# Optimization experiments

Hardware: AMD Instinct MI355X
Metric: run time of the kernel (lower is better)

The kernel has to match this reference:

```python
import jax, jax.numpy as jnp
import numpy as np

B, S, D = 2, 2048, 1024
H, DH = 16, 64
C = 64          # chunk_size (sliding window)
WF = 4          # widening factor
FMIN = jnp.finfo(jnp.float32).min


def _ln(x, scale, offset, eps=1e-5):
    mu = jnp.mean(x, axis=-1, keepdims=True)
    var = jnp.var(x, axis=-1, keepdims=True)
    return (x - mu) * jax.lax.rsqrt(var + eps) * scale + offset


def setup_inputs() -> dict:
    key = jax.random.key(0)
    ks = jax.random.split(key, 12)
    std = 0.02
    inp = {
        'x': jax.random.normal(ks[0], (B, S, D), dtype=jnp.float32),
        'causal_mask': jnp.tril(jnp.ones((S, S), dtype=bool))[None, None],  # (1,1,S,S)
        'pos': jax.random.normal(ks[1], (C, D), dtype=jnp.float32),          # pos_0..pos_{C-1}
        'rpe': std * jax.random.normal(ks[2], (H, C), dtype=jnp.float32),
        'Wq': std * jax.random.normal(ks[3], (D, H * DH), dtype=jnp.float32),
        'Wk': std * jax.random.normal(ks[4], (D, H * DH), dtype=jnp.float32),
        'Wv': std * jax.random.normal(ks[5], (D, H * DH), dtype=jnp.float32),
        'Wo': std * jax.random.normal(ks[6], (H * DH, D), dtype=jnp.float32),
        'ln1_scale': jnp.ones((D,), jnp.float32),
        'ln1_offset': jnp.zeros((D,), jnp.float32),
        'W1': std * jax.random.normal(ks[7], (D, WF * D), dtype=jnp.float32),
        'b1': jnp.zeros((WF * D,), jnp.float32),
        'W2': std * jax.random.normal(ks[8], (WF * D, D), dtype=jnp.float32),
        'b2': jnp.zeros((D,), jnp.float32),
        'ln2_scale': jnp.ones((D,), jnp.float32),
        'ln2_offset': jnp.zeros((D,), jnp.float32),
    }
    return inp


def _sliding_window_mask(rpe, seq_len):
    # mask[h,t,T] = rpe[h, t-T] if 0 <= t-T < C (lower diagonals), else -inf
    d = jnp.arange(seq_len)[:, None] - jnp.arange(seq_len)[None, :]  # (S,S)
    valid = (d >= 0) & (d < C)
    dc = jnp.clip(d, 0, C - 1)
    val = jnp.where(valid[None], rpe[:, dc], 0.0)  # (H,S,S)
    return jnp.where(val != 0, val, FMIN)


def reference(x, causal_mask, pos, rpe, Wq, Wk, Wv, Wo, ln1_scale, ln1_offset,
              W1, b1, W2, b2, ln2_scale, ln2_offset):
    seq_len = x.shape[1]
    # front/rear positional vectors: pos_i added at positions i, i+C, i+2C, ...
    h = x + pos[jnp.arange(seq_len) % C]  # (B,S,D)

    q = (h @ Wq).reshape(B, seq_len, H, DH)
    k = (h @ Wk).reshape(B, seq_len, H, DH)
    v = (h @ Wv).reshape(B, seq_len, H, DH)

    attn = jnp.einsum('bthd,bThd->bhtT', q, k) * (1.0 / jnp.sqrt(DH))
    attn = attn + _sliding_window_mask(rpe, seq_len)[None]  # learned diag bias
    attn = jnp.where(causal_mask, attn, FMIN)
    attn = jax.nn.softmax(attn, axis=-1)

    out = jnp.einsum('bhtT,bThd->bthd', attn, v).reshape(B, seq_len, H * DH)
    out = out @ Wo

    # dropout_prob = 0 -> identity
    attention = _ln(h + out, ln1_scale, ln1_offset)
    ff = jax.nn.relu(attention @ W1 + b1) @ W2 + b2
    return _ln(ff + attention, ln2_scale, ln2_offset)
```

## Files before the change

### kernel.cpp

```cpp
#include <hip/hip_runtime.h>
#include <hip/hip_bf16.h>

#define DEVI static __device__ __forceinline__

typedef __attribute__((ext_vector_type(4))) float f32x4;
typedef __attribute__((ext_vector_type(8))) short bf16x8;
typedef __attribute__((ext_vector_type(4))) short s16x4;

constexpr int TB  = 2;
constexpr int TS  = 2048;
constexpr int TD  = 1024;
constexpr int TH  = 16;
constexpr int TDH = 64;
constexpr int TC  = 64;
constexpr int TFF = 4096;
constexpr int TM  = TB * TS;

DEVI float bf2f(short s) {
  return __builtin_bit_cast(float, (unsigned)((unsigned short)s) << 16);
}
DEVI short f2bf(float f) {
  return __builtin_bit_cast(short, __float2bfloat16(f));
}

#define GLD16(gp, lp)                                              \
  __builtin_amdgcn_global_load_lds(                                \
      (const __attribute__((address_space(1))) void*)(gp),         \
      (__attribute__((address_space(3))) void*)(lp), 16, 0, 0)

#define WAITVM(N) asm volatile("s_waitcnt vmcnt(" #N ")" ::: "memory")

__global__ __launch_bounds__(256) void k_trans_all(
    const float* __restrict__ Wq, const float* __restrict__ Wk,
    const float* __restrict__ Wv, const float* __restrict__ Wo,
    const float* __restrict__ W1, const float* __restrict__ W2,
    __hip_bfloat16* __restrict__ WqkvT, __hip_bfloat16* __restrict__ WoT,
    __hip_bfloat16* __restrict__ W1T, __hip_bfloat16* __restrict__ W2T) {
  __shared__ float tile[32][33];
  int bid = blockIdx.x;
  const float* src; __hip_bfloat16* dst;
  int K, N, n0, k0;
  if (bid < 4096) {
    int m = bid >> 10, t = bid & 1023;
    src = (m == 0) ? Wq : (m == 1) ? Wk : (m == 2) ? Wv : Wo;
    dst = (m == 3) ? WoT : WqkvT + (size_t)m * TD * TD;
    K = TD; N = TD; n0 = (t & 31) * 32; k0 = (t >> 5) * 32;
  } else if (bid < 8192) {
    int t = bid - 4096;
    src = W1; dst = W1T; K = TD; N = TFF;
    n0 = (t & 127) * 32; k0 = (t >> 7) * 32;
  } else {
    int t = bid - 8192;
    src = W2; dst = W2T; K = TFF; N = TD;
    n0 = (t & 31) * 32; k0 = (t >> 5) * 32;
  }
  int tx = threadIdx.x & 31, ty = threadIdx.x >> 5;
  for (int i = 0; i < 32; i += 8)
    tile[ty + i][tx] = src[(size_t)(k0 + ty + i) * N + n0 + tx];
  __syncthreads();
  for (int i = 0; i < 32; i += 8)
    dst[(size_t)(n0 + ty + i) * K + k0 + tx] = __float2bfloat16(tile[tx][ty + i]);
}

__global__ __launch_bounds__(256) void k_addpos(
    const float* __restrict__ x, const float* __restrict__ pos,
    __hip_bfloat16* __restrict__ hb, int total4) {
  int i = blockIdx.x * 256 + threadIdx.x;
  if (i >= total4) return;
  int e = i * 4;
  int d = e & (TD - 1);
  int t = (e / TD) & (TS - 1);
  f32x4 xv = *(const f32x4*)(x + e);
  f32x4 pv = *(const f32x4*)(pos + (size_t)(t & (TC - 1)) * TD + d);
  s16x4 hb4;
  for (int j = 0; j < 4; j++) hb4[j] = f2bf(xv[j] + pv[j]);
  *(s16x4*)((short*)hb + e) = hb4;
}

template <int BN, int EPI>
__global__ __launch_bounds__(512, 2) void k_gemm8(
    const __hip_bfloat16* __restrict__ A, const __hip_bfloat16* __restrict__ BT,
    void* __restrict__ Cout, const float* __restrict__ bias,
    int M, int N, int K, int lda, int ldb) {
  constexpr int BM = 256, BK = 32;
  constexpr int FN = BN / 64;
  __shared__ __align__(16) short As[4][BM * BK];
  __shared__ __align__(16) short Bs[4][BN * BK];
  int tid = threadIdx.x, lane = tid & 63, wave = tid >> 6;
  int wm = wave >> 2, wn = wave & 3;
  int fr = lane & 15, fg = lane >> 4;
  int m0 = blockIdx.x * BM, n0 = blockIdx.y * BN;
  size_t koff = (size_t)blockIdx.z * K;
  const short* Ab = (const short*)A + koff;
  const short* Bb = (const short*)BT + koff;

  int r0 = tid >> 2, s0 = (tid & 3) ^ ((r0 >> 1) & 3);
  int r1 = 128 + r0, s1 = (tid & 3) ^ ((r1 >> 1) & 3);
  const short* pA0 = Ab + (size_t)(m0 + r0) * lda + s0 * 8;
  const short* pA1 = Ab + (size_t)(m0 + r1) * lda + s1 * 8;
  const short* pB0 = Bb + (size_t)(n0 + r0) * ldb + s0 * 8;
  const short* pB1 = (BN == 256) ? Bb + (size_t)(n0 + r1) * ldb + s1 * 8 : pB0;
  int dst0 = (wave * 64) * 16;
  int dst1 = (512 + wave * 64) * 16;

  auto stageA = [&](int d, int T) {
    GLD16(pA0 + T * BK, (char*)&As[d][0] + dst0);
    GLD16(pA1 + T * BK, (char*)&As[d][0] + dst1);
  };
  auto stageB = [&](int d, int T) {
    GLD16(pB0 + T * BK, (char*)&Bs[d][0] + dst0);
    if constexpr (BN == 256) GLD16(pB1 + T * BK, (char*)&Bs[d][0] + dst1);
  };

  f32x4 acc[8][FN];
#pragma unroll
  for (int m = 0; m < 8; m++)
#pragma unroll
    for (int n = 0; n < FN; n++) acc[m][n] = f32x4{0.f, 0.f, 0.f, 0.f};

  const int nt = K / BK;
  stageA(0, 0); stageB(0, 0);
  stageA(1, 1); stageB(1, 1);
  stageA(2, 2); stageB(2, 2);
  if (BN == 256) { WAITVM(8); } else { WAITVM(6); }
  __builtin_amdgcn_s_barrier();

  for (int t = 0; t < nt; t++) {
    int d = t & 3, pf = (t + 3) & 3;
    bool dopf = (t + 3) < nt;
    const char* Al = (const char*)&As[d][0];
    const char* Bl = (const char*)&Bs[d][0];
    if constexpr (BN == 256) {
      bf16x8 a[4], b[4];
#pragma unroll
      for (int mt = 0; mt < 4; mt++) {
        int row = wm * 128 + mt * 16 + fr;
        a[mt] = *(const bf16x8*)(Al + row * 64 + ((fg ^ ((row >> 1) & 3)) << 4));
      }
#pragma unroll
      for (int n = 0; n < 4; n++) {
        int row = wn * 64 + n * 16 + fr;
        b[n] = *(const bf16x8*)(Bl + row * 64 + ((fg ^ ((row >> 1) & 3)) << 4));
      }
      if (dopf) stageA(pf, t + 3);
      __builtin_amdgcn_s_barrier();
      __builtin_amdgcn_s_setprio(1);
#pragma unroll
      for (int mt = 0; mt < 4; mt++)
#pragma unroll
        for (int n = 0; n < 4; n++)
          acc[mt][n] = __builtin_amdgcn_mfma_f32_16x16x32_bf16(a[mt], b[n],
                                                               acc[mt][n], 0, 0, 0);
      __builtin_amdgcn_s_setprio(0);
      __builtin_amdgcn_s_barrier();
#pragma unroll
      for (int mt = 0; mt < 4; mt++) {
        int row = wm * 128 + 64 + mt * 16 + fr;
        a[mt] = *(const bf16x8*)(Al + row * 64 + ((fg ^ ((row >> 1) & 3)) << 4));
      }
      if (dopf) stageB(pf, t + 3);
      if (t < nt - 3) { WAITVM(8); }
      else if (t == nt - 3) { WAITVM(4); }
      else if (t == nt - 2) { WAITVM(0); }
      __builtin_amdgcn_s_barrier();
      __builtin_amdgcn_s_setprio(1);
#pragma unroll
      for (int mt = 0; mt < 4; mt++)
#pragma unroll
        for (int n = 0; n < 4; n++)
          acc[4 + mt][n] = __builtin_amdgcn_mfma_f32_16x16x32_bf16(a[mt], b[n],
                                                                   acc[4 + mt][n], 0, 0, 0);
      __builtin_amdgcn_s_setprio(0);
      __builtin_amdgcn_s_barrier();
    } else {
      bf16x8 a[8], b[2];
#pragma unroll
      for (int mt = 0; mt < 8; mt++) {
        int row = wm * 128 + mt * 16 + fr;
        a[mt] = *(const bf16x8*)(Al + row * 64 + ((fg ^ ((row >> 1) & 3)) << 4));
      }
#pragma unroll
      for (int n = 0; n < 2; n++) {
        int row = wn * 32 + n * 16 + fr;
        b[n] = *(const bf16x8*)(Bl + row * 64 + ((fg ^ ((row >> 1) & 3)) << 4));
      }
      if (dopf) { stageA(pf, t + 3); stageB(pf, t + 3); }
      if (t < nt - 3) { WAITVM(6); }
      else if (t == nt - 3) { WAITVM(3); }
      else if (t == nt - 2) { WAITVM(0); }
      __builtin_amdgcn_s_barrier();
      __builtin_amdgcn_s_setprio(1);
#pragma unroll
      for (int mt = 0; mt < 8; mt++)
#pragma unroll
        for (int n = 0; n < 2; n++)
          acc[mt][n] = __builtin_amdgcn_mfma_f32_16x16x32_bf16(a[mt], b[n],
                                                               acc[mt][n], 0, 0, 0);
      __builtin_amdgcn_s_setprio(0);
      __builtin_amdgcn_s_barrier();
    }
  }

  float* Cf = (float*)Cout + (size_t)blockIdx.z * M * N;
#pragma unroll
  for (int mt = 0; mt < 8; mt++)
#pragma unroll
    for (int n = 0; n < FN; n++) {
      int col = n0 + wn * (BN / 4) + n * 16 + fr;
      float bv = (EPI == 1) ? bias[col] : 0.f;
#pragma unroll
      for (int j = 0; j < 4; j++) {
        int row = m0 + wm * 128 + mt * 16 + fg * 4 + j;
        float v = acc[mt][n][j];
        if (EPI == 1) { v += bv; v = fmaxf(v, 0.f); }
        if (EPI == 2)
          Cf[(size_t)row * N + col] = v;
        else
          ((__hip_bfloat16*)Cout)[(size_t)row * N + col] = __float2bfloat16(v);
      }
    }
}

__global__ __launch_bounds__(256) void k_vtrans(
    const __hip_bfloat16* __restrict__ qkv, __hip_bfloat16* __restrict__ vT) {
  __shared__ short tile[64][68];
  int bh = blockIdx.x;
  int tb = blockIdx.y;
  int b = bh >> 4, h = bh & 15;
  int tid = threadIdx.x;
#pragma unroll
  for (int i = 0; i < 2; i++) {
    int c = i * 256 + tid;
    int trow = c >> 3, seg = c & 7;
    bf16x8 v = *(const bf16x8*)((const short*)qkv +
        (size_t)(b * TS + tb * 64 + trow) * 3072 + 2048 + h * TDH + seg * 8);
    s16x4 lo = {v[0], v[1], v[2], v[3]}, hi = {v[4], v[5], v[6], v[7]};
    *(s16x4*)&tile[trow][seg * 8] = lo;
    *(s16x4*)&tile[trow][seg * 8 + 4] = hi;
  }
  __syncthreads();
#pragma unroll
  for (int i2 = 0; i2 < 2; i2++) {
    int c = i2 * 256 + tid;
    int d = c >> 3, ts = c & 7;
    bf16x8 o;
#pragma unroll
    for (int j = 0; j < 8; j++) o[j] = tile[ts * 8 + j][d];
    *(bf16x8*)((short*)vT + (size_t)bh * TDH * TS + (size_t)d * TS +
               tb * 64 + ts * 8) = o;
  }
}

__global__ __launch_bounds__(256) void k_attn(
    const __hip_bfloat16* __restrict__ qkv, const __hip_bfloat16* __restrict__ vT,
    const float* __restrict__ rpe, __hip_bfloat16* __restrict__ out) {
  __shared__ __align__(16) short K_lds[128 * 64];
  __shared__ __align__(16) short VT_lds[64 * 128];
  __shared__ __align__(16) short P_lds[4][16 * 136];
  __shared__ float rpe_lds[TC];
  int tid = threadIdx.x, lane = tid & 63, wave = tid >> 6;
  int fr = lane & 15, g = lane >> 4;
  int blk = blockIdx.x;
  int qt = blk & 31, bh = blk >> 5;
  int h = bh & 15, b = bh >> 4;
  int t0 = qt * 64;
  const short* qg = (const short*)qkv;

  if (tid < TC) rpe_lds[tid] = rpe[h * TC + tid];

#pragma unroll
  for (int i = 0; i < 4; i++) {
    int cb = i * 256 + wave * 64;
    int c = cb + lane;
    int row = c >> 3, slot = c & 7;
    int seg = slot ^ (row & 7);
    int kr = t0 - 64 + row; if (kr < 0) kr = 0;
    GLD16(qg + ((size_t)(b * TS + kr) * 3072 + 1024 + h * TDH + seg * 8),
          (char*)K_lds + cb * 16);
  }
  const short* vg = (const short*)vT + (size_t)bh * TDH * TS;
#pragma unroll
  for (int i = 0; i < 4; i++) {
    int cb = i * 256 + wave * 64;
    int c = cb + lane;
    int row = c >> 4, slot = c & 15;
    int seg = slot ^ (row & 15);
    int tc = t0 - 64 + seg * 8; if (tc < 0) tc = 0;
    GLD16(vg + (size_t)row * TS + tc, (char*)VT_lds + cb * 16);
  }

  int qrow = t0 + wave * 16 + fr;
  const short* qptr = qg + ((size_t)(b * TS + qrow) * 3072 + h * TDH + g * 8);
  bf16x8 qf0 = *(const bf16x8*)qptr;
  bf16x8 qf1 = *(const bf16x8*)(qptr + 32);

  __syncthreads();

  f32x4 S[8] = {};
#pragma unroll
  for (int kk = 0; kk < 2; kk++) {
    bf16x8 a = kk ? qf1 : qf0;
#pragma unroll
    for (int nt = 0; nt < 8; nt++) {
      int row = nt * 16 + fr;
      int slot = (kk * 4 + g) ^ (row & 7);
      bf16x8 bfrag = *(const bf16x8*)((const char*)K_lds + row * 128 + slot * 16);
      S[nt] = __builtin_amdgcn_mfma_f32_16x16x32_bf16(a, bfrag, S[nt], 0, 0, 0);
    }
  }

  int wq = wave * 16;
#pragma unroll
  for (int r = 0; r < 4; r++) {
    int ql = g * 4 + r;
    float sc[8];
    float m = -3.4028235e38f;
#pragma unroll
    for (int nt = 0; nt < 8; nt++) {
      int jj = nt * 16 + fr;
      int d = wq + ql + 64 - jj;
      bool valid = (d >= 0) && (d < TC) && (t0 - 64 + jj >= 0);
      float v = valid ? (S[nt][r] * 0.125f + rpe_lds[d & (TC - 1)])
                      : -3.4028235e38f;
      sc[nt] = v;
      m = fmaxf(m, v);
    }
#pragma unroll
    for (int o = 1; o < 16; o <<= 1) m = fmaxf(m, __shfl_xor(m, o));
    float p[8], sum = 0.f;
#pragma unroll
    for (int nt = 0; nt < 8; nt++) { p[nt] = __expf(sc[nt] - m); sum += p[nt]; }
#pragma unroll
    for (int o = 1; o < 16; o <<= 1) sum += __shfl_xor(sum, o);
    float rs = 1.0f / sum;
#pragma unroll
    for (int nt = 0; nt < 8; nt++)
      P_lds[wave][ql * 136 + nt * 16 + fr] = f2bf(p[nt] * rs);
  }

  f32x4 O[4] = {};
#pragma unroll
  for (int kk = 0; kk < 4; kk++) {
    bf16x8 pa = *(const bf16x8*)((const char*)&P_lds[wave][0] +
                                 fr * 272 + kk * 64 + g * 16);
#pragma unroll
    for (int dt = 0; dt < 4; dt++) {
      int row = dt * 16 + fr;
      int slot = (kk * 4 + g) ^ (row & 15);
      bf16x8 vb = *(const bf16x8*)((const char*)VT_lds + row * 256 + slot * 16);
      O[dt] = __builtin_amdgcn_mfma_f32_16x16x32_bf16(pa, vb, O[dt], 0, 0, 0);
    }
  }

  size_t ob = ((size_t)(b * TS + t0 + wq + g * 4)) * TD + h * TDH;
#pragma unroll
  for (int dt = 0; dt < 4; dt++)
#pragma unroll
    for (int r = 0; r < 4; r++)
      ((short*)out)[ob + (size_t)r * TD + dt * 16 + fr] = f2bf(O[dt][r]);
}

DEVI float block_sum(float v, float* red) {
  for (int o = 32; o; o >>= 1) v += __shfl_xor(v, o);
  int wave = threadIdx.x >> 6;
  if ((threadIdx.x & 63) == 0) red[wave] = v;
  __syncthreads();
  float r = red[0] + red[1] + red[2] + red[3];
  __syncthreads();
  return r;
}

__global__ __launch_bounds__(256) void k_ln1(
    const float* __restrict__ x, const float* __restrict__ pos,
    const float* __restrict__ P0, const float* __restrict__ P1,
    const float* __restrict__ scale, const float* __restrict__ offset,
    float* __restrict__ outf, __hip_bfloat16* __restrict__ outb) {
  __shared__ float red[4];
  int row = blockIdx.x, tid = threadIdx.x;
  int t = row & (TS - 1), pr = t & (TC - 1);
  size_t base = (size_t)row * TD + tid * 4;
  f32x4 xv = *(const f32x4*)(x + base);
  f32x4 pv = *(const f32x4*)(pos + (size_t)pr * TD + tid * 4);
  f32x4 a0 = *(const f32x4*)(P0 + base);
  f32x4 a1 = *(const f32x4*)(P1 + base);
  xv = xv + pv + a0 + a1;
  float s = xv[0] + xv[1] + xv[2] + xv[3];
  s = block_sum(s, red);
  float mu = s * (1.f / TD);
  float s2 = 0.f;
  for (int j = 0; j < 4; j++) { float dlt = xv[j] - mu; s2 += dlt * dlt; }
  s2 = block_sum(s2, red);
  float rs = rsqrtf(s2 * (1.f / TD) + 1e-5f);
  f32x4 sc = *(const f32x4*)(scale + tid * 4);
  f32x4 of = *(const f32x4*)(offset + tid * 4);
  f32x4 y;
  for (int j = 0; j < 4; j++) y[j] = (xv[j] - mu) * rs * sc[j] + of[j];
  *(f32x4*)(outf + base) = y;
  s16x4 pb;
  for (int j = 0; j < 4; j++) pb[j] = f2bf(y[j]);
  *(s16x4*)((short*)outb + base) = pb;
}

__global__ __launch_bounds__(256) void k_ln2(
    const float* __restrict__ P0, const float* __restrict__ P1,
    const float* __restrict__ R, const float* __restrict__ bias,
    const float* __restrict__ scale, const float* __restrict__ offset,
    float* __restrict__ outf) {
  __shared__ float red[4];
  int row = blockIdx.x, tid = threadIdx.x;
  size_t base = (size_t)row * TD + tid * 4;
  f32x4 a0 = *(const f32x4*)(P0 + base);
  f32x4 a1 = *(const f32x4*)(P1 + base);
  f32x4 rv = *(const f32x4*)(R + base);
  f32x4 bi = *(const f32x4*)(bias + tid * 4);
  f32x4 xv = a0 + a1 + rv + bi;
  float s = xv[0] + xv[1] + xv[2] + xv[3];
  s = block_sum(s, red);
  float mu = s * (1.f / TD);
  float s2 = 0.f;
  for (int j = 0; j < 4; j++) { float dlt = xv[j] - mu; s2 += dlt * dlt; }
  s2 = block_sum(s2, red);
  float rs = rsqrtf(s2 * (1.f / TD) + 1e-5f);
  f32x4 sc = *(const f32x4*)(scale + tid * 4);
  f32x4 of = *(const f32x4*)(offset + tid * 4);
  f32x4 y;
  for (int j = 0; j < 4; j++) y[j] = (xv[j] - mu) * rs * sc[j] + of[j];
  *(f32x4*)(outf + base) = y;
}

extern "C" void kernel_launch(void* const* d_in, const int* in_sizes, int n_in,
                              void* d_out, int out_size, void* d_ws, size_t ws_size,
                              hipStream_t stream) {
  const float* x    = (const float*)d_in[0];
  const float* pos  = (const float*)d_in[2];
  const float* rpe  = (const float*)d_in[3];
  const float* Wq   = (const float*)d_in[4];
  const float* Wk   = (const float*)d_in[5];
  const float* Wv   = (const float*)d_in[6];
  const float* Wo   = (const float*)d_in[7];
  const float* ln1s = (const float*)d_in[8];
  const float* ln1o = (const float*)d_in[9];
  const float* W1   = (const float*)d_in[10];
  const float* b1   = (const float*)d_in[11];
  const float* W2   = (const float*)d_in[12];
  const float* b2   = (const float*)d_in[13];
  const float* ln2s = (const float*)d_in[14];
  const float* ln2o = (const float*)d_in[15];

  char* ws = (char*)d_ws;
  const size_t MB = 1ull << 20;
  __hip_bfloat16* WqkvT = (__hip_bfloat16*)(ws + 0 * MB);
  __hip_bfloat16* WoT   = (__hip_bfloat16*)(ws + 6 * MB);
  __hip_bfloat16* W1T   = (__hip_bfloat16*)(ws + 8 * MB);
  __hip_bfloat16* W2T   = (__hip_bfloat16*)(ws + 16 * MB);
  __hip_bfloat16* hB    = (__hip_bfloat16*)(ws + 24 * MB);
  __hip_bfloat16* qkv   = (__hip_bfloat16*)(ws + 32 * MB);
  __hip_bfloat16* aoB   = (__hip_bfloat16*)(ws + 56 * MB);
  float*          oF2   = (float*)(ws + 64 * MB);
  float*          atF   = (float*)(ws + 96 * MB);
  __hip_bfloat16* atB   = (__hip_bfloat16*)(ws + 24 * MB);
  __hip_bfloat16* ff1   = (__hip_bfloat16*)(ws + 32 * MB);
  float*          ff2   = (float*)(ws + 64 * MB);
  __hip_bfloat16* vTb   = (__hip_bfloat16*)(ws + 112 * MB);

  dim3 blk(256), blk5(512);

  k_trans_all<<<12288, blk, 0, stream>>>(Wq, Wk, Wv, Wo, W1, W2,
                                         WqkvT, WoT, W1T, W2T);

  k_addpos<<<(TM * TD / 4 + 255) / 256, blk, 0, stream>>>(x, pos, hB, TM * TD / 4);

  k_gemm8<256, 0><<<dim3(TM / 256, 3072 / 256, 1), blk5, 0, stream>>>(
      hB, WqkvT, qkv, nullptr, TM, 3072, TD, TD, TD);

  k_vtrans<<<dim3(TB * TH, TS / 64), blk, 0, stream>>>(qkv, vTb);
  k_attn<<<TB * TH * (TS / 64), blk, 0, stream>>>(qkv, vTb, rpe, aoB);

  k_gemm8<128, 2><<<dim3(TM / 256, TD / 128, 2), blk5, 0, stream>>>(
      aoB, WoT, oF2, nullptr, TM, TD, TD / 2, TD, TD);

  k_ln1<<<TM, blk, 0, stream>>>(x, pos, oF2, oF2 + (size_t)TM * TD, ln1s, ln1o, atF, atB);

  k_gemm8<256, 1><<<dim3(TM / 256, TFF / 256, 1), blk5, 0, stream>>>(
      atB, W1T, ff1, b1, TM, TFF, TD, TD, TD);

  k_gemm8<128, 2><<<dim3(TM / 256, TD / 128, 2), blk5, 0, stream>>>(
      ff1, W2T, ff2, nullptr, TM, TD, TFF / 2, TFF, TFF);

  k_ln2<<<TM, blk, 0, stream>>>(ff2, ff2 + (size_t)TM * TD, atF, b2, ln2s, ln2o,
                                (float*)d_out);
}
```

Measured before the change: 204.9 us.

## Restructure GEMM main loop with one barrier per tile and B-fragment double buffering

Rewrites the bf16 MFMA GEMM pipeline so each K-tile needs one barrier instead of two or three. B fragments for the next tile are read from LDS into registers ahead of time while the current tile computes. Prefetch issue is now unified and happens after the barrier. For BN=128 the wave grid changes from 2x4 to 4x2 (64x64 per wave) to balance A and B fragment reuse. The extra live registers for the next B fragments could raise pressure under the 512-thread, 2-block launch bound.

After: 238.7 us. 16.5% more time.

```diff
diff --git a/kernel.cpp b/kernel.cpp
--- a/kernel.cpp
+++ b/kernel.cpp
@@ -78,16 +78,18 @@
 }
 
 template <int BN, int EPI>
-__global__ __launch_bounds__(512, 2) void k_gemm8(
+__global__ __launch_bounds__(512, 2) void k_gemm9(
     const __hip_bfloat16* __restrict__ A, const __hip_bfloat16* __restrict__ BT,
     void* __restrict__ Cout, const float* __restrict__ bias,
     int M, int N, int K, int lda, int ldb) {
   constexpr int BM = 256, BK = 32;
-  constexpr int FN = BN / 64;
+  constexpr int MT  = (BN == 256) ? 8 : 4;
+  constexpr int WMR = (BN == 256) ? 128 : 64;
   __shared__ __align__(16) short As[4][BM * BK];
   __shared__ __align__(16) short Bs[4][BN * BK];
   int tid = threadIdx.x, lane = tid & 63, wave = tid >> 6;
-  int wm = wave >> 2, wn = wave & 3;
+  int wm = (BN == 256) ? (wave >> 2) : (wave >> 1);
+  int wn = (BN == 256) ? (wave & 3) : (wave & 1);
   int fr = lane & 15, fg = lane >> 4;
   int m0 = blockIdx.x * BM, n0 = blockIdx.y * BN;
   size_t koff = (size_t)blockIdx.z * K;
@@ -103,114 +105,84 @@
   int dst0 = (wave * 64) * 16;
   int dst1 = (512 + wave * 64) * 16;
 
-  auto stageA = [&](int d, int T) {
+  auto stage = [&](int d, int T) {
     GLD16(pA0 + T * BK, (char*)&As[d][0] + dst0);
     GLD16(pA1 + T * BK, (char*)&As[d][0] + dst1);
-  };
-  auto stageB = [&](int d, int T) {
     GLD16(pB0 + T * BK, (char*)&Bs[d][0] + dst0);
     if constexpr (BN == 256) GLD16(pB1 + T * BK, (char*)&Bs[d][0] + dst1);
   };
-
-  f32x4 acc[8][FN];
-#pragma unroll
-  for (int m = 0; m < 8; m++)
-#pragma unroll
-    for (int n = 0; n < FN; n++) acc[m][n] = f32x4{0.f, 0.f, 0.f, 0.f};
+  auto readB = [&](int d, bf16x8* b) {
+#pragma unroll
+    for (int n = 0; n < 4; n++) {
+      int row = wn * 64 + n * 16 + fr;
+      b[n] = *(const bf16x8*)((const char*)&Bs[d][0] + row * 64 +
+                              ((fg ^ ((row >> 1) & 3)) << 4));
+    }
+  };
+
+  f32x4 acc[MT][4];
+#pragma unroll
+  for (int m = 0; m < MT; m++)
+#pragma unroll
+    for (int n = 0; n < 4; n++) acc[m][n] = f32x4{0.f, 0.f, 0.f, 0.f};
 
   const int nt = K / BK;
-  stageA(0, 0); stageB(0, 0);
-  stageA(1, 1); stageB(1, 1);
-  stageA(2, 2); stageB(2, 2);
-  if (BN == 256) { WAITVM(8); } else { WAITVM(6); }
+  stage(0, 0);
+  stage(1, 1);
+  if (BN == 256) { WAITVM(4); } else { WAITVM(3); }
   __builtin_amdgcn_s_barrier();
+  asm volatile("" ::: "memory");
+  stage(2, 2);
+
+  bf16x8 bcur[4], bnxt[4];
+  readB(0, bcur);
 
   for (int t = 0; t < nt; t++) {
-    int d = t & 3, pf = (t + 3) & 3;
-    bool dopf = (t + 3) < nt;
-    const char* Al = (const char*)&As[d][0];
-    const char* Bl = (const char*)&Bs[d][0];
-    if constexpr (BN == 256) {
-      bf16x8 a[4], b[4];
+    const char* Al = (const char*)&As[t & 3][0];
+    if (t + 1 < nt) {
+      if (t + 2 < nt) {
+        if (BN == 256) { WAITVM(4); } else { WAITVM(3); }
+      } else {
+        WAITVM(0);
+      }
+      __builtin_amdgcn_s_barrier();
+      asm volatile("" ::: "memory");
+      if (t + 3 < nt) stage((t + 3) & 3, t + 3);
+      readB((t + 1) & 3, bnxt);
+    }
+#pragma unroll
+    for (int h = 0; h < MT / 4; h++) {
+      bf16x8 af[4];
 #pragma unroll
       for (int mt = 0; mt < 4; mt++) {
-        int row = wm * 128 + mt * 16 + fr;
-        a[mt] = *(const bf16x8*)(Al + row * 64 + ((fg ^ ((row >> 1) & 3)) << 4));
+        int row = wm * WMR + h * 64 + mt * 16 + fr;
+        af[mt] = *(const bf16x8*)(Al + row * 64 + ((fg ^ ((row >> 1) & 3)) << 4));
       }
-#pragma unroll
-      for (int n = 0; n < 4; n++) {
-        int row = wn * 64 + n * 16 + fr;
-        b[n] = *(const bf16x8*)(Bl + row * 64 + ((fg ^ ((row >> 1) & 3)) << 4));
-      }
-      if (dopf) stageA(pf, t + 3);
-      __builtin_amdgcn_s_barrier();
       __builtin_amdgcn_s_setprio(1);
 #pragma unroll
       for (int mt = 0; mt < 4; mt++)
 #pragma unroll
         for (int n = 0; n < 4; n++)
-          acc[mt][n] = __builtin_amdgcn_mfma_f32_16x16x32_bf16(a[mt], b[n],
-                                                               acc[mt][n], 0, 0, 0);
+          acc[h * 4 + mt][n] = __builtin_amdgcn_mfma_f32_16x16x32_bf16(
+              af[mt], bcur[n], acc[h * 4 + mt][n], 0, 0, 0);
       __builtin_amdgcn_s_setprio(0);
-      __builtin_amdgcn_s_barrier();
-#pragma unroll
-      for (int mt = 0; mt < 4; mt++) {
-        int row = wm * 128 + 64 + mt * 16 + fr;
-        a[mt] = *(const bf16x8*)(Al + row * 64 + ((fg ^ ((row >> 1) & 3)) << 4));
-      }
-      if (dopf) stageB(pf, t + 3);
-      if (t < nt - 3) { WAITVM(8); }
-      else if (t == nt - 3) { WAITVM(4); }
-      else if (t == nt - 2) { WAITVM(0); }
-      __builtin_amdgcn_s_barrier();
-      __builtin_amdgcn_s_setprio(1);
-#pragma unroll
-      for (int mt = 0; mt < 4; mt++)
-#pragma unroll
-        for (int n = 0; n < 4; n++)
-          acc[4 + mt][n] = __builtin_amdgcn_mfma_f32_16x16x32_bf16(a[mt], b[n],
-                                                                   acc[4 + mt][n], 0, 0, 0);
-      __builtin_amdgcn_s_setprio(0);
-      __builtin_amdgcn_s_barrier();
-    } else {
-      bf16x8 a[8], b[2];
-#pragma unroll
-      for (int mt = 0; mt < 8; mt++) {
-        int row = wm * 128 + mt * 16 + fr;
-        a[mt] = *(const bf16x8*)(Al + row * 64 + ((fg ^ ((row >> 1) & 3)) << 4));
-      }
-#pragma unroll
-      for (int n = 0; n < 2; n++) {
-        int row = wn * 32 + n * 16 + fr;
-        b[n] = *(const bf16x8*)(Bl + row * 64 + ((fg ^ ((row >> 1) & 3)) << 4));
-      }
-      if (dopf) { stageA(pf, t + 3); stageB(pf, t + 3); }
-      if (t < nt - 3) { WAITVM(6); }
-      else if (t == nt - 3) { WAITVM(3); }
-      else if (t == nt - 2) { WAITVM(0); }
-      __builtin_amdgcn_s_barrier();
-      __builtin_amdgcn_s_setprio(1);
-#pragma unroll
-      for (int mt = 0; mt < 8; mt++)
-#pragma unroll
-        for (int n = 0; n < 2; n++)
-          acc[mt][n] = __builtin_amdgcn_mfma_f32_16x16x32_bf16(a[mt], b[n],
-                                                               acc[mt][n], 0, 0, 0);
-      __builtin_amdgcn_s_setprio(0);
-      __builtin_amdgcn_s_barrier();
+    }
+    if (t + 1 < nt) {
+#pragma unroll
+      for (int n = 0; n < 4; n++) bcur[n] = bnxt[n];
     }
   }
 
   float* Cf = (float*)Cout + (size_t)blockIdx.z * M * N;
 #pragma unroll
-  for (int mt = 0; mt < 8; mt++)
-#pragma unroll
-    for (int n = 0; n < FN; n++) {
-      int col = n0 + wn * (BN / 4) + n * 16 + fr;
+  for (int mt = 0; mt < MT; mt++)
+#pragma unroll
+    for (int n = 0; n < 4; n++) {
+      int col = n0 + wn * 64 + n * 16 + fr;
       float bv = (EPI == 1) ? bias[col] : 0.f;
 #pragma unroll
       for (int j = 0; j < 4; j++) {
-        int row = m0 + wm * 128 + mt * 16 + fg * 4 + j;
+        int row = m0 + wm * WMR + (mt >> 2) * 64 + (mt & 3) * 16 + fg * 4 + j;
         float v = acc[mt][n][j];
         if (EPI == 1) { v += bv; v = fmaxf(v, 0.f); }
         if (EPI == 2)
@@ -470,21 +442,21 @@
 
   k_addpos<<<(TM * TD / 4 + 255) / 256, blk, 0, stream>>>(x, pos, hB, TM * TD / 4);
 
-  k_gemm8<256, 0><<<dim3(TM / 256, 3072 / 256, 1), blk5, 0, stream>>>(
+  k_gemm9<256, 0><<<dim3(TM / 256, 3072 / 256, 1), blk5, 0, stream>>>(
       hB, WqkvT, qkv, nullptr, TM, 3072, TD, TD, TD);
 
   k_vtrans<<<dim3(TB * TH, TS / 64), blk, 0, stream>>>(qkv, vTb);
   k_attn<<<TB * TH * (TS / 64), blk, 0, stream>>>(qkv, vTb, rpe, aoB);
 
-  k_gemm8<128, 2><<<dim3(TM / 256, TD / 128, 2), blk5, 0, stream>>>(
+  k_gemm9<128, 2><<<dim3(TM / 256, TD / 128, 2), blk5, 0, stream>>>(
       aoB, WoT, oF2, nullptr, TM, TD, TD / 2, TD, TD);
 
   k_ln1<<<TM, blk, 0, stream>>>(x, pos, oF2, oF2 + (size_t)TM * TD, ln1s, ln1o, atF, atB);
 
-  k_gemm8<256, 1><<<dim3(TM / 256, TFF / 256, 1), blk5, 0, stream>>>(
+  k_gemm9<256, 1><<<dim3(TM / 256, TFF / 256, 1), blk5, 0, stream>>>(
       atB, W1T, ff1, b1, TM, TFF, TD, TD, TD);
 
-  k_gemm8<128, 2><<<dim3(TM / 256, TD / 128, 2), blk5, 0, stream>>>(
+  k_gemm9<128, 2><<<dim3(TM / 256, TD / 128, 2), blk5, 0, stream>>>(
       ff1, W2T, ff2, nullptr, TM, TD, TFF / 2, TFF, TFF);
 
   k_ln2<<<TM, blk, 0, stream>>>(ff2, ff2 + (size_t)TM * TD, atF, b2, ln2s, ln2o,
```
